# Kernel tuning notes

Hardware: AMD Instinct MI355X
Metric: run time of the kernel (lower is better)

## Reference

```python
import jax, jax.numpy as jnp
import numpy as np

K_REP = 4          # repulsion neighbors
REP_THRESH = 0.02  # repulsion distance threshold
K_NORM = 16        # PCA-normal neighborhood size (includes self)
CD_W, REP_W, NORM_W = 1.0, 0.1, 0.01


def _pdist2(x, y):
    # squared pairwise distances: [B,N,M]
    xx = (x * x).sum(-1)
    yy = (y * y).sum(-1)
    return xx[..., :, None] + yy[..., None, :] - 2.0 * jnp.einsum('bnd,bmd->bnm', x, y)


def _gather_points(pts, idx):
    # pts: [B,N,3], idx: [B,N,k] -> [B,N,k,3]
    return jax.vmap(lambda p, i: p[i])(pts, idx)


def _pca_normals(pts):
    # normals via PCA over K_NORM nearest neighbors (self included)
    D = _pdist2(pts, pts)                       # [B,N,N]
    _, idx = jax.lax.top_k(-D, K_NORM)          # [B,N,K]
    nb = _gather_points(pts, idx)               # [B,N,K,3]
    c = nb - nb.mean(axis=-2, keepdims=True)
    cov = jnp.einsum('bnkd,bnke->bnde', c, c) / K_NORM  # [B,N,3,3]
    _, vecs = jnp.linalg.eigh(cov)              # ascending eigenvalues
    return vecs[..., :, 0]                      # eigenvector of smallest eigenvalue


def reference(pred, gt):
    # --- chamfer distance (squared, bidirectional mean) ---
    Dpg = _pdist2(pred, gt)                     # [B,N,M]
    cd = Dpg.min(axis=-1).mean() + Dpg.min(axis=-2).mean()

    # --- repulsion loss: k=4 NN on pred (excluding self) ---
    Dpp = _pdist2(pred, pred)                   # [B,N,N]
    neg_d2, _ = jax.lax.top_k(-Dpp, K_REP + 1)  # nearest incl. self
    d2 = -neg_d2[..., 1:]                       # drop self
    d = jnp.sqrt(jnp.maximum(d2, 1e-12))
    rep = jax.nn.relu(REP_THRESH - d).mean()

    # --- normal consistency via PCA normals (k=16) ---
    n_pred = _pca_normals(pred)
    n_gt = _pca_normals(gt)
    normc = 1.0 - (n_pred * n_gt).sum(-1).mean()

    return CD_W * cd + REP_W * rep + NORM_W * normc


def setup_inputs() -> dict:
    key = jax.random.key(0)
    k1, k2 = jax.random.split(key)
    B, N = 8, 2048
    pred = jax.random.uniform(k1, (B, N, 3), dtype=jnp.float32)
    gt = jax.random.uniform(k2, (B, N, 3), dtype=jnp.float32)
    return {"pred": pred, "gt": gt}
```

## Files before the change

kernel.cpp:

```cpp
#include <hip/hip_runtime.h>


#define NB 8
#define NP 2048
#define KW 10
#define KN 16


__device__ __forceinline__ float f_slapy2(float x, float y) {
    float xa = fabsf(x), ya = fabsf(y);
    float w = fmaxf(xa, ya), zm = fminf(xa, ya);
    if (zm == 0.f) return w;
    float q = zm / w;
    return w * sqrtf(1.f + q * q);
}

__device__ __forceinline__ void f_slartg(float f, float g, float* cs, float* sn, float* r) {
    if (g == 0.f) { *cs = 1.f; *sn = 0.f; *r = f; }
    else if (f == 0.f) { *cs = 0.f; *sn = copysignf(1.f, g); *r = fabsf(g); }
    else {
        float d = sqrtf(__fadd_rn(__fmul_rn(f, f), __fmul_rn(g, g)));
        *cs = fabsf(f) / d;
        *r  = copysignf(d, f);
        *sn = g / *r;
    }
}

__device__ void f_slaev2(float a, float b, float c,
                         float* rt1, float* rt2, float* cs1, float* sn1) {
    float sm = a + c;
    float df = a - c;
    float adf = fabsf(df);
    float tb = b + b;
    float ab = fabsf(tb);
    float acmx, acmn;
    if (fabsf(a) > fabsf(c)) { acmx = a; acmn = c; } else { acmx = c; acmn = a; }
    float rt;
    if (adf > ab)      { float q = ab / adf; rt = adf * sqrtf(1.f + q * q); }
    else if (adf < ab) { float q = adf / ab; rt = ab * sqrtf(1.f + q * q); }
    else               rt = ab * sqrtf(2.f);
    int sgn1;
    if (sm < 0.f) {
        *rt1 = 0.5f * (sm - rt); sgn1 = -1;
        *rt2 = (acmx / *rt1) * acmn - (b / *rt1) * b;
    } else if (sm > 0.f) {
        *rt1 = 0.5f * (sm + rt); sgn1 = 1;
        *rt2 = (acmx / *rt1) * acmn - (b / *rt1) * b;
    } else {
        *rt1 = 0.5f * rt; *rt2 = -0.5f * rt; sgn1 = 1;
    }
    float cs; int sgn2;
    if (df >= 0.f) { cs = df + rt; sgn2 = 1; }
    else           { cs = df - rt; sgn2 = -1; }
    float acs = fabsf(cs);
    if (acs > ab) {
        float ct = -tb / cs;
        *sn1 = 1.f / sqrtf(1.f + ct * ct);
        *cs1 = ct * *sn1;
    } else {
        if (ab == 0.f) { *cs1 = 1.f; *sn1 = 0.f; }
        else {
            float tn = -cs / tb;
            *cs1 = 1.f / sqrtf(1.f + tn * tn);
            *sn1 = tn * *cs1;
        }
    }
    if (sgn1 == sgn2) { float tn = *cs1; *cs1 = -*sn1; *sn1 = tn; }
}

__device__ void ssyevd3_evec0(float a00, float a10, float a20,
                              float a11, float a21, float a22,
                              float* ox, float* oy, float* oz) {
    float d[3], e[2];
    float tau = 0.f, v2 = 0.f;
    float xnorm = fabsf(a20);
    if (xnorm == 0.f) {
        tau = 0.f;
        d[0] = a00; d[1] = a11; d[2] = a22; e[0] = a10; e[1] = a21;
    } else {
        float beta = -copysignf(f_slapy2(a10, xnorm), a10);
        tau = (beta - a10) / beta;
        float inv = 1.f / (a10 - beta);
        v2 = a20 * inv;
        float x1 = tau * (a11 + a21 * v2);
        float x2 = tau * (a21 + a22 * v2);
        float alpha = -0.5f * tau * (x1 + x2 * v2);
        float w1 = x1 + alpha;
        float w2 = x2 + alpha * v2;
        float b11 = a11 - 2.f * w1;
        float b21 = a21 - v2 * w1 - w2;
        float b22 = a22 - 2.f * (v2 * w2);
        d[0] = a00; d[1] = b11; d[2] = b22; e[0] = beta; e[1] = b21;
    }
    const float eps    = 5.9604645e-08f;
    const float eps2   = eps * eps;
    const float safmin = 1.1754944e-38f;
    const float ssfmax = sqrtf(1.f / safmin) / 3.f;
    const float ssfmin = sqrtf(safmin) / eps2;
    const int n = 3, nmaxit = 90;
    float z[3][3] = {{1.f,0.f,0.f},{0.f,1.f,0.f},{0.f,0.f,1.f}};
    int jtot = 0;
    int l1 = 1;

    while (true) {
        if (l1 > n) break;
        if (l1 > 1) e[l1 - 2] = 0.f;
        int m = n;
        for (int mi = l1; mi <= n - 1; ++mi) {
            float tst = fabsf(e[mi - 1]);
            if (tst == 0.f) { m = mi; break; }
            if (tst <= (sqrtf(fabsf(d[mi - 1])) * sqrtf(fabsf(d[mi]))) * eps) {
                e[mi - 1] = 0.f; m = mi; break;
            }
        }
        int l = l1, lsv = l, lend = m, lendsv = lend;
        l1 = m + 1;
        if (lend == l) continue;

        float anorm = 0.f;
        for (int i = l; i <= lend; ++i) anorm = fmaxf(anorm, fabsf(d[i - 1]));
        for (int i = l; i <= lend - 1; ++i) anorm = fmaxf(anorm, fabsf(e[i - 1]));
        int iscale = 0; float sclto = 1.f;
        if (anorm == 0.f) continue;
        if (anorm > ssfmax) { iscale = 1; sclto = ssfmax; }
        else if (anorm < ssfmin) { iscale = 2; sclto = ssfmin; }
        if (iscale) {
            float mul = sclto / anorm;
            for (int i = l; i <= lend; ++i) d[i - 1] *= mul;
            for (int i = l; i <= lend - 1; ++i) e[i - 1] *= mul;
        }
        if (fabsf(d[lend - 1]) < fabsf(d[l - 1])) { lend = lsv; l = lendsv; }

        if (lend > l) {
            while (true) {
                int mq = lend;
                if (l != lend) {
                    for (int i = l; i <= lend - 1; ++i) {
                        float ei = e[i - 1];
                        float tst = ei * ei;
                        if (tst <= (eps2 * fabsf(d[i - 1])) * fabsf(d[i]) + safmin) { mq = i; break; }
                    }
                }
                if (mq < lend) e[mq - 1] = 0.f;
                float p = d[l - 1];
                if (mq == l) { d[l - 1] = p; l = l + 1; if (l <= lend) continue; break; }
                if (mq == l + 1) {
                    float rt1, rt2, c, s;
                    f_slaev2(d[l - 1], e[l - 1], d[l], &rt1, &rt2, &c, &s);
                    for (int i = 0; i < 3; ++i) {
                        float temp = z[i][l];
                        z[i][l]     = c * temp - s * z[i][l - 1];
                        z[i][l - 1] = s * temp + c * z[i][l - 1];
                    }
                    d[l - 1] = rt1; d[l] = rt2; e[l - 1] = 0.f;
                    l += 2; if (l <= lend) continue; break;
                }
                if (jtot == nmaxit) break;
                jtot++;
                float g = (d[l] - p) / (2.f * e[l - 1]);
                float r = f_slapy2(g, 1.f);
                g = d[mq - 1] - p + e[l - 1] / (g + copysignf(r, g));
                float s = 1.f, c = 1.f; p = 0.f;
                float cw[2], sw[2];
                for (int i = mq - 1; i >= l; --i) {
                    float f = s * e[i - 1];
                    float b = c * e[i - 1];
                    f_slartg(g, f, &c, &s, &r);
                    if (i != mq - 1) e[i] = r;
                    g = d[i] - p;
                    r = (d[i - 1] - g) * s + 2.f * c * b;
                    p = s * r;
                    d[i] = g + p;
                    g = c * r - b;
                    cw[i - l] = c; sw[i - l] = -s;
                }
                for (int j = mq - l; j >= 1; --j) {
                    float cj = cw[j - 1], sj = sw[j - 1];
                    int c0 = l - 1 + (j - 1);
                    for (int i = 0; i < 3; ++i) {
                        float temp = z[i][c0 + 1];
                        z[i][c0 + 1] = cj * temp - sj * z[i][c0];
                        z[i][c0]     = sj * temp + cj * z[i][c0];
                    }
                }
                d[l - 1] -= p;
                e[l - 1] = g;
            }
        } else {
            while (true) {
                int mq = lend;
                if (l != lend) {
                    for (int i = l; i >= lend + 1; --i) {
                        float ei = e[i - 2];
                        float tst = ei * ei;
                        if (tst <= (eps2 * fabsf(d[i - 1])) * fabsf(d[i - 2]) + safmin) { mq = i; break; }
                    }
                }
                if (mq > lend) e[mq - 2] = 0.f;
                float p = d[l - 1];
                if (mq == l) { d[l - 1] = p; l = l - 1; if (l >= lend) continue; break; }
                if (mq == l - 1) {
                    float rt1, rt2, c, s;
                    f_slaev2(d[l - 2], e[l - 2], d[l - 1], &rt1, &rt2, &c, &s);
                    for (int i = 0; i < 3; ++i) {
                        float temp = z[i][l - 1];
                        z[i][l - 1] = c * temp - s * z[i][l - 2];
                        z[i][l - 2] = s * temp + c * z[i][l - 2];
                    }
                    d[l - 2] = rt1; d[l - 1] = rt2; e[l - 2] = 0.f;
                    l -= 2; if (l >= lend) continue; break;
                }
                if (jtot == nmaxit) break;
                jtot++;
                float g = (d[l - 2] - p) / (2.f * e[l - 2]);
                float r = f_slapy2(g, 1.f);
                g = d[mq - 1] - p + e[l - 2] / (g + copysignf(r, g));
                float s = 1.f, c = 1.f; p = 0.f;
                float cw[2], sw[2];
                for (int i = mq; i <= l - 1; ++i) {
                    float f = s * e[i - 1];
                    float b = c * e[i - 1];
                    f_slartg(g, f, &c, &s, &r);
                    if (i != mq) e[i - 2] = r;
                    g = d[i - 1] - p;
                    r = (d[i] - g) * s + 2.f * c * b;
                    p = s * r;
                    d[i - 1] = g + p;
                    g = c * r - b;
                    cw[i - mq] = c; sw[i - mq] = s;
                }
                for (int j = 1; j <= l - mq; ++j) {
                    float cj = cw[j - 1], sj = sw[j - 1];
                    int c0 = mq - 1 + (j - 1);
                    for (int i = 0; i < 3; ++i) {
                        float temp = z[i][c0 + 1];
                        z[i][c0 + 1] = cj * temp - sj * z[i][c0];
                        z[i][c0]     = sj * temp + cj * z[i][c0];
                    }
                }
                d[l - 1] -= p;
                e[l - 2] = g;
            }
        }
        if (iscale) {
            float mul = anorm / sclto;
            for (int i = lsv; i <= lendsv; ++i) d[i - 1] *= mul;
            for (int i = lsv; i <= lendsv - 1; ++i) e[i - 1] *= mul;
        }
        if (jtot >= nmaxit) break;
    }

    for (int ii = 2; ii <= 3; ++ii) {
        int i = ii - 1, k = i;
        float p = d[i - 1];
        for (int j = ii; j <= 3; ++j) if (d[j - 1] < p) { k = j; p = d[j - 1]; }
        if (k != i) {
            d[k - 1] = d[i - 1]; d[i - 1] = p;
            for (int r = 0; r < 3; ++r) { float t = z[r][i - 1]; z[r][i - 1] = z[r][k - 1]; z[r][k - 1] = t; }
        }
    }
    float r0 = z[0][0], r1 = z[1][0], r2 = z[2][0];
    if (tau != 0.f) {
        float sum = r1 + v2 * r2;
        r1 -= tau * sum;
        r2 -= tau * (v2 * sum);
    }
    *ox = r0; *oy = r1; *oz = r2;
}


__device__ __forceinline__ float dot_rn(float ax, float ay, float az,
                                        float bx, float by, float bz) {
    return __fadd_rn(__fadd_rn(__fmul_rn(ax, bx), __fmul_rn(ay, by)), __fmul_rn(az, bz));
}

__device__ __forceinline__ void chain10(unsigned k[KW], unsigned x) {
    unsigned t = x;
    #pragma unroll
    for (int s = 0; s < KW; ++s) {
        unsigned lo = k[s] < t ? k[s] : t;
        unsigned hi = k[s] < t ? t : k[s];
        k[s] = lo; t = hi;
    }
}
__device__ __forceinline__ void chain16(unsigned k[KN], unsigned x) {
    unsigned t = x;
    #pragma unroll
    for (int s = 0; s < KN; ++s) {
        unsigned lo = k[s] < t ? k[s] : t;
        unsigned hi = k[s] < t ? t : k[s];
        k[s] = lo; t = hi;
    }
}

#define KIDX(s, w, l) (((s) * 8 + (w)) * 64 + (l))

__global__ __launch_bounds__(512) void scan_kernel(
    const float* __restrict__ pred, const float* __restrict__ gt,
    float* __restrict__ nP, float* __restrict__ nG, double* __restrict__ acc)
{
    __shared__ float4 sHome[NP];
    __shared__ float4 sOther[NP];
    unsigned* kbuf = (unsigned*)sOther;
    float* mbuf = (float*)((char*)sOther + 20480);
    float* cache = (float*)sOther;

    int bi = blockIdx.x;
    bool predHome = bi < NB * 32;
    int lb = predHome ? bi : bi - NB * 32;
    int b = lb >> 5;
    int tile = lb & 31;
    int tid  = threadIdx.x;
    int wave = tid >> 6;
    int lane = tid & 63;

    const float* home  = (predHome ? pred : gt) + (size_t)b * NP * 3;
    const float* other = (predHome ? gt : pred) + (size_t)b * NP * 3;

    for (int t = tid; t < NP; t += 512) {
        float hx = home[3 * t], hy = home[3 * t + 1], hz = home[3 * t + 2];
        sHome[t] = make_float4(hx, hy, hz, dot_rn(hx, hy, hz, hx, hy, hz));
        float ox = other[3 * t], oy = other[3 * t + 1], oz = other[3 * t + 2];
        sOther[t] = make_float4(ox, oy, oz, 0.f);
    }
    __syncthreads();

    int im = tile * 64 + lane;
    float4 q = sHome[im];
    float qx = q.x, qy = q.y, qz = q.z, qq = q.w;

    unsigned keys[KW];
    #pragma unroll
    for (int s = 0; s < KW; ++s) keys[s] = 0x7F800000u | (unsigned)s;

    float minv = 1e30f;

    for (int t = 0; t < NP / 8; ++t) {
        int jj = (t << 3) | wave;
        float4 h = sHome[jj];
        float dotj = dot_rn(qx, qy, qz, h.x, h.y, h.z);
        float d2 = __fsub_rn(__fadd_rn(qq, h.w), __fmul_rn(2.f, dotj));
        chain10(keys, (__float_as_uint(d2) & 0xFFFFF800u) | (unsigned)jj);
        float4 o = sOther[jj];
        float ex = qx - o.x, ey = qy - o.y, ez = qz - o.z;
        minv = fminf(minv, fmaf(ex, ex, fmaf(ey, ey, ez * ez)));
    }
    __syncthreads();

    #pragma unroll
    for (int s = 0; s < KW; ++s) kbuf[KIDX(s, wave, lane)] = keys[s];
    mbuf[wave * 64 + lane] = minv;
    __syncthreads();

    if (wave != 0) return;

    unsigned k16[KN];
    #pragma unroll
    for (int s = 0; s < KW; ++s) k16[s] = keys[s];
    #pragma unroll
    for (int s = KW; s < KN; ++s) k16[s] = 0x7F800000u | (unsigned)s;
    for (int w = 1; w < 8; ++w) {
        #pragma unroll
        for (int s = 0; s < KW; ++s) chain16(k16, kbuf[KIDX(s, w, lane)]);
    }
    minv = fminf(fminf(fminf(mbuf[lane], mbuf[64 + lane]),
                       fminf(mbuf[128 + lane], mbuf[192 + lane])),
                 fminf(fminf(mbuf[256 + lane], mbuf[320 + lane]),
                       fminf(mbuf[384 + lane], mbuf[448 + lane])));

    unsigned flags = 0;
    #pragma unroll
    for (int w = 0; w < 8; ++w)
        flags |= (kbuf[KIDX(KW - 1, w, lane)] < k16[15]) ? (1u << w) : 0u;

    if (__any(flags != 0)) {
        #pragma unroll
        for (int s = 0; s < KN; ++s)
            k16[s] = flags ? (0x7F800000u | (unsigned)s) : k16[s];
        for (int w = 0; w < 8; ++w) {
            #pragma unroll
            for (int s = 0; s < KW; ++s) {
                unsigned kk = kbuf[KIDX(s, w, lane)];
                bool use = (flags != 0) && !((flags >> w) & 1);
                chain16(k16, use ? kk : 0xFFFFFFFFu);
            }
        }
        for (int w = 0; w < 8; ++w) {
            if (__any((flags >> w) & 1)) {
                bool actw = ((flags >> w) & 1) != 0;
                for (int t = 0; t < NP / 8; ++t) {
                    int jj = (t << 3) | w;
                    float4 h = sHome[jj];
                    float dotj = dot_rn(qx, qy, qz, h.x, h.y, h.z);
                    float d2 = __fsub_rn(__fadd_rn(qq, h.w), __fmul_rn(2.f, dotj));
                    unsigned key = (__float_as_uint(d2) & 0xFFFFF800u) | (unsigned)jj;
                    chain16(k16, actw ? key : 0xFFFFFFFFu);
                }
            }
        }
    }

    float rep = 0.0f;
    if (predHome) {
        #pragma unroll
        for (int r = 1; r <= 4; ++r) {
            float d2 = __uint_as_float(k16[r] & 0xFFFFF800u);
            float dd = sqrtf(fmaxf(d2, 1e-12f));
            rep += fmaxf(0.02f - dd, 0.0f);
        }
    }

    float sx = 0.f, sy = 0.f, sz = 0.f;
    #pragma unroll
    for (int s = 0; s < KN; ++s) {
        const float* hp = home + 3 * (size_t)(k16[s] & 0x7FFu);
        float px = hp[0], py = hp[1], pz = hp[2];
        cache[(s * 3 + 0) * 64 + lane] = px;
        cache[(s * 3 + 1) * 64 + lane] = py;
        cache[(s * 3 + 2) * 64 + lane] = pz;
        sx += px; sy += py; sz += pz;
    }
    float mx = sx * (1.0f / KN), my = sy * (1.0f / KN), mz = sz * (1.0f / KN);
    float cxx = 0.f, cxy = 0.f, cxz = 0.f, cyy = 0.f, cyz = 0.f, czz = 0.f;
    #pragma unroll
    for (int s = 0; s < KN; ++s) {
        float ax = cache[(s * 3 + 0) * 64 + lane] - mx;
        float ay = cache[(s * 3 + 1) * 64 + lane] - my;
        float az = cache[(s * 3 + 2) * 64 + lane] - mz;
        cxx += ax * ax; cxy += ax * ay; cxz += ax * az;
        cyy += ay * ay; cyz += ay * az; czz += az * az;
    }
    cxx *= (1.f / KN); cxy *= (1.f / KN); cxz *= (1.f / KN);
    cyy *= (1.f / KN); cyz *= (1.f / KN); czz *= (1.f / KN);

    float nx, ny, nz;
    ssyevd3_evec0(cxx, cxy, cxz, cyy, cyz, czz, &nx, &ny, &nz);

    float* nout = predHome ? nP : nG;
    int gi = b * NP + im;
    nout[gi * 3 + 0] = nx;
    nout[gi * 3 + 1] = ny;
    nout[gi * 3 + 2] = nz;

    double part = (double)minv * (1.0 / (NB * NP))
                + (double)rep  * (0.1 / (NB * NP * 4));

    #pragma unroll
    for (int off = 32; off > 0; off >>= 1) part += __shfl_down(part, off);
    if (lane == 0) atomicAdd(acc, part);
}

__global__ __launch_bounds__(1024) void dotfin_kernel(
    const float* __restrict__ nP, const float* __restrict__ nG,
    const double* __restrict__ acc, float* __restrict__ out)
{
    int tid = threadIdx.x;
    float s = 0.f;
    for (int i = tid; i < NB * NP; i += 1024)
        s += nP[3 * i] * nG[3 * i] + nP[3 * i + 1] * nG[3 * i + 1] + nP[3 * i + 2] * nG[3 * i + 2];
    double part = (double)s;
    #pragma unroll
    for (int off = 32; off > 0; off >>= 1) part += __shfl_down(part, off);
    __shared__ double w[16];
    if ((tid & 63) == 0) w[tid >> 6] = part;
    __syncthreads();
    if (tid == 0) {
        double t = 0.0;
        for (int k = 0; k < 16; ++k) t += w[k];
        out[0] = (float)(acc[0] - t * (0.01 / (NB * NP)) + 0.01);
    }
}

extern "C" void kernel_launch(void* const* d_in, const int* in_sizes, int n_in,
                              void* d_out, int out_size, void* d_ws, size_t ws_size,
                              hipStream_t stream)
{
    const float* pred = (const float*)d_in[0];
    const float* gt   = (const float*)d_in[1];

    char* base = (char*)d_ws;
    double* acc = (double*)base;
    float* nP = (float*)(base + 64);
    float* nG = nP + (size_t)NB * NP * 3;

    hipMemsetAsync(d_ws, 0, 64, stream);
    scan_kernel<<<dim3(NB * 32 * 2), dim3(512), 0, stream>>>(pred, gt, nP, nG, acc);
    dotfin_kernel<<<dim3(1), dim3(1024), 0, stream>>>(nP, nG, acc, (float*)d_out);
}
```

Before: 169.1 us.

## Prepack points into float4 buffers and read them directly instead of via LDS

Adds a repack kernel that converts pred/gt into float4 arrays with the squared norm precomputed. The scan kernel then drops its per-block LDS staging of home and other points and reads wave-uniform float4 values straight from global memory, using readfirstlane so the loads become scalar/broadcast. This shrinks LDS use, which may allow more resident blocks, and removes the redundant per-block staging. Normals are stored as float4 for aligned writes and reads in the final reduction. The cost is an extra kernel launch and inner-loop loads that now depend on cache hits rather than LDS.

```diff
diff --git a/kernel.cpp b/kernel.cpp
--- a/kernel.cpp
+++ b/kernel.cpp
@@ -278,8 +278,9 @@
     unsigned t = x;
     #pragma unroll
     for (int s = 0; s < KW; ++s) {
-        unsigned lo = k[s] < t ? k[s] : t;
-        unsigned hi = k[s] < t ? t : k[s];
+        unsigned a = k[s];
+        unsigned lo = a < t ? a : t;
+        unsigned hi = a < t ? t : a;
         k[s] = lo; t = hi;
     }
 }
@@ -287,23 +288,36 @@
     unsigned t = x;
     #pragma unroll
     for (int s = 0; s < KN; ++s) {
-        unsigned lo = k[s] < t ? k[s] : t;
-        unsigned hi = k[s] < t ? t : k[s];
+        unsigned a = k[s];
+        unsigned lo = a < t ? a : t;
+        unsigned hi = a < t ? t : a;
         k[s] = lo; t = hi;
     }
+}
+
+__global__ __launch_bounds__(256) void repack_kernel(
+    const float* __restrict__ pred, const float* __restrict__ gt,
+    float4* __restrict__ p4, float4* __restrict__ g4)
+{
+    int i = blockIdx.x * 256 + threadIdx.x;
+    int half = NB * NP;
+    const float* src = (i < half) ? pred : gt;
+    int k = (i < half) ? i : i - half;
+    float x = src[3 * k], y = src[3 * k + 1], z = src[3 * k + 2];
+    float4 v = make_float4(x, y, z, dot_rn(x, y, z, x, y, z));
+    ((i < half) ? p4 : g4)[k] = v;
 }
 
 #define KIDX(s, w, l) (((s) * 8 + (w)) * 64 + (l))
 
 __global__ __launch_bounds__(512) void scan_kernel(
     const float* __restrict__ pred, const float* __restrict__ gt,
-    float* __restrict__ nP, float* __restrict__ nG, double* __restrict__ acc)
+    const float4* __restrict__ p4, const float4* __restrict__ g4,
+    float4* __restrict__ nP4, float4* __restrict__ nG4, double* __restrict__ acc)
 {
-    __shared__ float4 sHome[NP];
-    __shared__ float4 sOther[NP];
-    unsigned* kbuf = (unsigned*)sOther;
-    float* mbuf = (float*)((char*)sOther + 20480);
-    float* cache = (float*)sOther;
+    __shared__ unsigned kbuf[KW * 8 * 64];
+    __shared__ float mbuf[8 * 64];
+    float* cache = (float*)kbuf;
 
     int bi = blockIdx.x;
     bool predHome = bi < NB * 32;
@@ -314,19 +328,14 @@
     int wave = tid >> 6;
     int lane = tid & 63;
 
-    const float* home  = (predHome ? pred : gt) + (size_t)b * NP * 3;
-    const float* other = (predHome ? gt : pred) + (size_t)b * NP * 3;
-
-    for (int t = tid; t < NP; t += 512) {
-        float hx = home[3 * t], hy = home[3 * t + 1], hz = home[3 * t + 2];
-        sHome[t] = make_float4(hx, hy, hz, dot_rn(hx, hy, hz, hx, hy, hz));
-        float ox = other[3 * t], oy = other[3 * t + 1], oz = other[3 * t + 2];
-        sOther[t] = make_float4(ox, oy, oz, 0.f);
-    }
-    __syncthreads();
+    const float*  home   = (predHome ? pred : gt) + (size_t)b * NP * 3;
+    const float4* home4  = (predHome ? p4 : g4) + (size_t)b * NP;
+    const float4* other4 = (predHome ? g4 : p4) + (size_t)b * NP;
+
+    int wv = __builtin_amdgcn_readfirstlane(wave);
 
     int im = tile * 64 + lane;
-    float4 q = sHome[im];
+    float4 q = home4[im];
     float qx = q.x, qy = q.y, qz = q.z, qq = q.w;
 
     unsigned keys[KW];
@@ -336,16 +345,15 @@
     float minv = 1e30f;
 
     for (int t = 0; t < NP / 8; ++t) {
-        int jj = (t << 3) | wave;
-        float4 h = sHome[jj];
+        int jj = (t << 3) | wv;
+        float4 h = home4[jj];
         float dotj = dot_rn(qx, qy, qz, h.x, h.y, h.z);
         float d2 = __fsub_rn(__fadd_rn(qq, h.w), __fmul_rn(2.f, dotj));
         chain10(keys, (__float_as_uint(d2) & 0xFFFFF800u) | (unsigned)jj);
-        float4 o = sOther[jj];
+        float4 o = other4[jj];
         float ex = qx - o.x, ey = qy - o.y, ez = qz - o.z;
         minv = fminf(minv, fmaf(ex, ex, fmaf(ey, ey, ez * ez)));
     }
-    __syncthreads();
 
     #pragma unroll
     for (int s = 0; s < KW; ++s) kbuf[KIDX(s, wave, lane)] = keys[s];
@@ -390,7 +398,7 @@
                 bool actw = ((flags >> w) & 1) != 0;
                 for (int t = 0; t < NP / 8; ++t) {
                     int jj = (t << 3) | w;
-                    float4 h = sHome[jj];
+                    float4 h = home4[jj];
                     float dotj = dot_rn(qx, qy, qz, h.x, h.y, h.z);
                     float d2 = __fsub_rn(__fadd_rn(qq, h.w), __fmul_rn(2.f, dotj));
                     unsigned key = (__float_as_uint(d2) & 0xFFFFF800u) | (unsigned)jj;
@@ -436,11 +444,8 @@
     float nx, ny, nz;
     ssyevd3_evec0(cxx, cxy, cxz, cyy, cyz, czz, &nx, &ny, &nz);
 
-    float* nout = predHome ? nP : nG;
     int gi = b * NP + im;
-    nout[gi * 3 + 0] = nx;
-    nout[gi * 3 + 1] = ny;
-    nout[gi * 3 + 2] = nz;
+    (predHome ? nP4 : nG4)[gi] = make_float4(nx, ny, nz, 0.f);
 
     double part = (double)minv * (1.0 / (NB * NP))
                 + (double)rep  * (0.1 / (NB * NP * 4));
@@ -451,13 +456,15 @@
 }
 
 __global__ __launch_bounds__(1024) void dotfin_kernel(
-    const float* __restrict__ nP, const float* __restrict__ nG,
+    const float4* __restrict__ nP4, const float4* __restrict__ nG4,
     const double* __restrict__ acc, float* __restrict__ out)
 {
     int tid = threadIdx.x;
     float s = 0.f;
-    for (int i = tid; i < NB * NP; i += 1024)
-        s += nP[3 * i] * nG[3 * i] + nP[3 * i + 1] * nG[3 * i + 1] + nP[3 * i + 2] * nG[3 * i + 2];
+    for (int i = tid; i < NB * NP; i += 1024) {
+        float4 a = nP4[i], c = nG4[i];
+        s += a.x * c.x + a.y * c.y + a.z * c.z;
+    }
     double part = (double)s;
     #pragma unroll
     for (int off = 32; off > 0; off >>= 1) part += __shfl_down(part, off);
@@ -480,10 +487,13 @@
 
     char* base = (char*)d_ws;
     double* acc = (double*)base;
-    float* nP = (float*)(base + 64);
-    float* nG = nP + (size_t)NB * NP * 3;
+    float4* p4  = (float4*)(base + 64);
+    float4* g4  = p4 + (size_t)NB * NP;
+    float4* nP4 = g4 + (size_t)NB * NP;
+    float4* nG4 = nP4 + (size_t)NB * NP;
 
     hipMemsetAsync(d_ws, 0, 64, stream);
-    scan_kernel<<<dim3(NB * 32 * 2), dim3(512), 0, stream>>>(pred, gt, nP, nG, acc);
-    dotfin_kernel<<<dim3(1), dim3(1024), 0, stream>>>(nP, nG, acc, (float*)d_out);
-}
+    repack_kernel<<<dim3(2 * NB * NP / 256), dim3(256), 0, stream>>>(pred, gt, p4, g4);
+    scan_kernel<<<dim3(NB * 32 * 2), dim3(512), 0, stream>>>(pred, gt, p4, g4, nP4, nG4, acc);
+    dotfin_kernel<<<dim3(1), dim3(1024), 0, stream>>>(nP4, nG4, acc, (float*)d_out);
+}
```

Result: slower. 207.7 us (+22.9%).

## Split scan into two key chains and spread merge/PCA across all waves

Applied to the files above, without the earlier changes.

The main scan loop now keeps two independent top-10 chains per thread, with strides j and j|8, so each iteration has more instruction-level parallelism. The merge, fallback rescan and PCA stage used to run on wave 0 only while the other seven waves exited. Each wave now handles 8 queries, replicated across its lanes, which spreads that serial tail over the whole block. The fallback rescan and PCA read point data from global memory instead of shared memory. Only lanes below 8 write results, so most lanes do redundant work, and the fallback path pays for global loads.

```diff
diff --git a/kernel.cpp b/kernel.cpp
--- a/kernel.cpp
+++ b/kernel.cpp
@@ -278,8 +278,9 @@
     unsigned t = x;
     #pragma unroll
     for (int s = 0; s < KW; ++s) {
-        unsigned lo = k[s] < t ? k[s] : t;
-        unsigned hi = k[s] < t ? t : k[s];
+        unsigned a = k[s];
+        unsigned lo = a < t ? a : t;
+        unsigned hi = a < t ? t : a;
         k[s] = lo; t = hi;
     }
 }
@@ -287,23 +288,24 @@
     unsigned t = x;
     #pragma unroll
     for (int s = 0; s < KN; ++s) {
-        unsigned lo = k[s] < t ? k[s] : t;
-        unsigned hi = k[s] < t ? t : k[s];
+        unsigned a = k[s];
+        unsigned lo = a < t ? a : t;
+        unsigned hi = a < t ? t : a;
         k[s] = lo; t = hi;
     }
 }
 
-#define KIDX(s, w, l) (((s) * 8 + (w)) * 64 + (l))
+#define KIDX(s, v, l) (((s) * 16 + (v)) * 64 + (l))
 
 __global__ __launch_bounds__(512) void scan_kernel(
     const float* __restrict__ pred, const float* __restrict__ gt,
     float* __restrict__ nP, float* __restrict__ nG, double* __restrict__ acc)
 {
-    __shared__ float4 sHome[NP];
-    __shared__ float4 sOther[NP];
-    unsigned* kbuf = (unsigned*)sOther;
-    float* mbuf = (float*)((char*)sOther + 20480);
-    float* cache = (float*)sOther;
+    __shared__ unsigned smem[16384];
+    float4* sHome  = (float4*)smem;
+    float4* sOther = (float4*)smem + NP;
+    unsigned* kbuf = smem;
+    float* mbuf = (float*)(smem + KW * 16 * 64);
 
     int bi = blockIdx.x;
     bool predHome = bi < NB * 32;
@@ -329,72 +331,85 @@
     float4 q = sHome[im];
     float qx = q.x, qy = q.y, qz = q.z, qq = q.w;
 
-    unsigned keys[KW];
-    #pragma unroll
-    for (int s = 0; s < KW; ++s) keys[s] = 0x7F800000u | (unsigned)s;
-
-    float minv = 1e30f;
-
-    for (int t = 0; t < NP / 8; ++t) {
-        int jj = (t << 3) | wave;
-        float4 h = sHome[jj];
-        float dotj = dot_rn(qx, qy, qz, h.x, h.y, h.z);
-        float d2 = __fsub_rn(__fadd_rn(qq, h.w), __fmul_rn(2.f, dotj));
-        chain10(keys, (__float_as_uint(d2) & 0xFFFFF800u) | (unsigned)jj);
-        float4 o = sOther[jj];
-        float ex = qx - o.x, ey = qy - o.y, ez = qz - o.z;
-        minv = fminf(minv, fmaf(ex, ex, fmaf(ey, ey, ez * ez)));
+    unsigned keysA[KW], keysB[KW];
+    #pragma unroll
+    for (int s = 0; s < KW; ++s) { keysA[s] = 0x7F800000u | (unsigned)s; keysB[s] = keysA[s]; }
+
+    float minvA = 1e30f, minvB = 1e30f;
+
+    for (int u = 0; u < NP / 16; ++u) {
+        int j0 = (u << 4) | wave;
+        int j1 = j0 | 8;
+        float4 h0 = sHome[j0];
+        float4 h1 = sHome[j1];
+        float d0 = dot_rn(qx, qy, qz, h0.x, h0.y, h0.z);
+        float d2a = __fsub_rn(__fadd_rn(qq, h0.w), __fmul_rn(2.f, d0));
+        chain10(keysA, (__float_as_uint(d2a) & 0xFFFFF800u) | (unsigned)j0);
+        float d1 = dot_rn(qx, qy, qz, h1.x, h1.y, h1.z);
+        float d2b = __fsub_rn(__fadd_rn(qq, h1.w), __fmul_rn(2.f, d1));
+        chain10(keysB, (__float_as_uint(d2b) & 0xFFFFF800u) | (unsigned)j1);
+        float4 o0 = sOther[j0];
+        float4 o1 = sOther[j1];
+        float ea = qx - o0.x, fa = qy - o0.y, ga = qz - o0.z;
+        minvA = fminf(minvA, fmaf(ea, ea, fmaf(fa, fa, ga * ga)));
+        float eb = qx - o1.x, fb = qy - o1.y, gb = qz - o1.z;
+        minvB = fminf(minvB, fmaf(eb, eb, fmaf(fb, fb, gb * gb)));
     }
     __syncthreads();
 
     #pragma unroll
-    for (int s = 0; s < KW; ++s) kbuf[KIDX(s, wave, lane)] = keys[s];
-    mbuf[wave * 64 + lane] = minv;
+    for (int s = 0; s < KW; ++s) {
+        kbuf[KIDX(s, wave, lane)]     = keysA[s];
+        kbuf[KIDX(s, wave + 8, lane)] = keysB[s];
+    }
+    mbuf[wave * 64 + lane] = fminf(minvA, minvB);
     __syncthreads();
 
-    if (wave != 0) return;
+    int lq = wave * 8 + (lane & 7);
+    bool writer = lane < 8;
 
     unsigned k16[KN];
     #pragma unroll
-    for (int s = 0; s < KW; ++s) k16[s] = keys[s];
-    #pragma unroll
-    for (int s = KW; s < KN; ++s) k16[s] = 0x7F800000u | (unsigned)s;
-    for (int w = 1; w < 8; ++w) {
+    for (int s = 0; s < KN; ++s) k16[s] = 0x7F800000u | (unsigned)s;
+    for (int v = 0; v < 16; ++v) {
         #pragma unroll
-        for (int s = 0; s < KW; ++s) chain16(k16, kbuf[KIDX(s, w, lane)]);
-    }
-    minv = fminf(fminf(fminf(mbuf[lane], mbuf[64 + lane]),
-                       fminf(mbuf[128 + lane], mbuf[192 + lane])),
-                 fminf(fminf(mbuf[256 + lane], mbuf[320 + lane]),
-                       fminf(mbuf[384 + lane], mbuf[448 + lane])));
+        for (int s = 0; s < KW; ++s) chain16(k16, kbuf[KIDX(s, v, lq)]);
+    }
+    float minv = mbuf[lq];
+    #pragma unroll
+    for (int w = 1; w < 8; ++w) minv = fminf(minv, mbuf[w * 64 + lq]);
 
     unsigned flags = 0;
     #pragma unroll
-    for (int w = 0; w < 8; ++w)
-        flags |= (kbuf[KIDX(KW - 1, w, lane)] < k16[15]) ? (1u << w) : 0u;
+    for (int v = 0; v < 16; ++v)
+        flags |= (kbuf[KIDX(KW - 1, v, lq)] < k16[15]) ? (1u << v) : 0u;
 
     if (__any(flags != 0)) {
         #pragma unroll
         for (int s = 0; s < KN; ++s)
             k16[s] = flags ? (0x7F800000u | (unsigned)s) : k16[s];
-        for (int w = 0; w < 8; ++w) {
+        for (int v = 0; v < 16; ++v) {
             #pragma unroll
             for (int s = 0; s < KW; ++s) {
-                unsigned kk = kbuf[KIDX(s, w, lane)];
-                bool use = (flags != 0) && !((flags >> w) & 1);
+                unsigned kk = kbuf[KIDX(s, v, lq)];
+                bool use = (flags != 0) && !((flags >> v) & 1);
                 chain16(k16, use ? kk : 0xFFFFFFFFu);
             }
         }
-        for (int w = 0; w < 8; ++w) {
-            if (__any((flags >> w) & 1)) {
-                bool actw = ((flags >> w) & 1) != 0;
-                for (int t = 0; t < NP / 8; ++t) {
-                    int jj = (t << 3) | w;
-                    float4 h = sHome[jj];
-                    float dotj = dot_rn(qx, qy, qz, h.x, h.y, h.z);
-                    float d2 = __fsub_rn(__fadd_rn(qq, h.w), __fmul_rn(2.f, dotj));
+        int gq = tile * 64 + lq;
+        float gqx = home[3 * gq], gqy = home[3 * gq + 1], gqz = home[3 * gq + 2];
+        float gqq = dot_rn(gqx, gqy, gqz, gqx, gqy, gqz);
+        for (int v = 0; v < 16; ++v) {
+            if (__any((flags >> v) & 1)) {
+                bool actv = ((flags >> v) & 1) != 0;
+                for (int u = 0; u < NP / 16; ++u) {
+                    int jj = (u << 4) | v;
+                    float hx = home[3 * jj], hy = home[3 * jj + 1], hz = home[3 * jj + 2];
+                    float hw = dot_rn(hx, hy, hz, hx, hy, hz);
+                    float dj = dot_rn(gqx, gqy, gqz, hx, hy, hz);
+                    float d2 = __fsub_rn(__fadd_rn(gqq, hw), __fmul_rn(2.f, dj));
                     unsigned key = (__float_as_uint(d2) & 0xFFFFF800u) | (unsigned)jj;
-                    chain16(k16, actw ? key : 0xFFFFFFFFu);
+                    chain16(k16, actv ? key : 0xFFFFFFFFu);
                 }
             }
         }
@@ -414,19 +429,14 @@
     #pragma unroll
     for (int s = 0; s < KN; ++s) {
         const float* hp = home + 3 * (size_t)(k16[s] & 0x7FFu);
-        float px = hp[0], py = hp[1], pz = hp[2];
-        cache[(s * 3 + 0) * 64 + lane] = px;
-        cache[(s * 3 + 1) * 64 + lane] = py;
-        cache[(s * 3 + 2) * 64 + lane] = pz;
-        sx += px; sy += py; sz += pz;
+        sx += hp[0]; sy += hp[1]; sz += hp[2];
     }
     float mx = sx * (1.0f / KN), my = sy * (1.0f / KN), mz = sz * (1.0f / KN);
     float cxx = 0.f, cxy = 0.f, cxz = 0.f, cyy = 0.f, cyz = 0.f, czz = 0.f;
     #pragma unroll
     for (int s = 0; s < KN; ++s) {
-        float ax = cache[(s * 3 + 0) * 64 + lane] - mx;
-        float ay = cache[(s * 3 + 1) * 64 + lane] - my;
-        float az = cache[(s * 3 + 2) * 64 + lane] - mz;
+        const float* hp = home + 3 * (size_t)(k16[s] & 0x7FFu);
+        float ax = hp[0] - mx, ay = hp[1] - my, az = hp[2] - mz;
         cxx += ax * ax; cxy += ax * ay; cxz += ax * az;
         cyy += ay * ay; cyz += ay * az; czz += az * az;
     }
@@ -436,15 +446,16 @@
     float nx, ny, nz;
     ssyevd3_evec0(cxx, cxy, cxz, cyy, cyz, czz, &nx, &ny, &nz);
 
-    float* nout = predHome ? nP : nG;
-    int gi = b * NP + im;
-    nout[gi * 3 + 0] = nx;
-    nout[gi * 3 + 1] = ny;
-    nout[gi * 3 + 2] = nz;
-
-    double part = (double)minv * (1.0 / (NB * NP))
-                + (double)rep  * (0.1 / (NB * NP * 4));
-
+    if (writer) {
+        float* nout = predHome ? nP : nG;
+        int gi = b * NP + tile * 64 + lq;
+        nout[gi * 3 + 0] = nx;
+        nout[gi * 3 + 1] = ny;
+        nout[gi * 3 + 2] = nz;
+    }
+
+    double part = writer ? ((double)minv * (1.0 / (NB * NP))
+                          + (double)rep  * (0.1 / (NB * NP * 4))) : 0.0;
     #pragma unroll
     for (int off = 32; off > 0; off >>= 1) part += __shfl_down(part, off);
     if (lane == 0) atomicAdd(acc, part);
```

New measurement: 210.4 us. 24.4% more time.
